# Optimization experiments

Measured on AMD Instinct MI355X. Metric: run time of the kernel, lower is better.

Reference implementation:

```python
import jax, jax.numpy as jnp
import numpy as np

EPS = 1e-8

def setup_inputs() -> dict:
    key = jax.random.key(0)
    k1, k2 = jax.random.split(key)
    B, IN, OUT, G = 32768, 256, 256, 5
    x = jax.random.normal(k1, (B, IN), dtype=jnp.float32)
    grid = jnp.linspace(-1.0, 1.0, G).astype(jnp.float32)
    coef = jax.random.normal(k2, (OUT, IN, G), dtype=jnp.float32) * 0.1
    scale = jnp.ones((OUT, IN), dtype=jnp.float32)
    bias = jnp.zeros((OUT,), dtype=jnp.float32)
    return {"x": x, "grid": grid, "coef": coef, "scale": scale, "bias": bias}

def reference(x, grid, coef, scale, bias):
    # global min-max normalization to [-1, 1]
    xmin, xmax = x.min(), x.max()
    xn = 2.0 * (x - xmin) / (xmax - xmin + EPS) - 1.0
    # cubic bump B-spline-like basis: (batch, in, grid)
    dist = jnp.abs(xn[..., None] - grid)
    basis = jnp.where(dist < 1.0, 1.0 - dist ** 3, 0.0)
    basis = basis / (basis.sum(axis=-1, keepdims=True) + EPS)
    # fused contraction over (in, grid); equals ((basis*coef).sum(-1)*scale).sum(-1)
    w = coef * scale[..., None]          # (out, in, grid)
    out = jnp.einsum('big,oig->bo', basis, w) + bias
    return out
```

## Files before the change

kernel.cpp:

```cpp
#include <hip/hip_runtime.h>
#include <stdint.h>


#define B_SZ   32768
#define IN_SZ  256
#define OUT_SZ 256
#define EPSF   1e-8f

typedef __bf16 bf16x8 __attribute__((ext_vector_type(8)));
typedef unsigned short ushort8 __attribute__((ext_vector_type(8)));
typedef float floatx16 __attribute__((ext_vector_type(16)));

union frag_u { uint4 u; bf16x8 v; };

__device__ __forceinline__ unsigned short f2bf(float f) {
  unsigned u = __float_as_uint(f);
  u += 0x7FFFu + ((u >> 16) & 1u);
  return (unsigned short)(u >> 16);
}


__global__ void __launch_bounds__(256) prep_kernel(const float* __restrict__ coef,
                                                   const float* __restrict__ scale,
                                                   const float* __restrict__ x,
                                                   unsigned short* __restrict__ wf,
                                                   float* __restrict__ part, int n4) {
  const int t = threadIdx.x;
  if (blockIdx.x < 256) {
    int idx = blockIdx.x * 256 + t;
    int o = idx >> 8, i = idx & 255;
    float s = scale[idx];
    const float* c = coef + (size_t)idx * 5;
    ushort8 v;
    v[0] = f2bf(c[0] * s); v[1] = f2bf(c[1] * s); v[2] = f2bf(c[2] * s);
    v[3] = f2bf(c[3] * s); v[4] = f2bf(c[4] * s);
    v[5] = 0; v[6] = 0; v[7] = 0;
    int chunk = (((o >> 5) * 64 + (i >> 2)) * 2 + ((i >> 1) & 1)) * 64
                + (i & 1) * 32 + (o & 31);
    *(ushort8*)(wf + (size_t)chunk * 8) = v;
  } else {
    int mb = blockIdx.x - 256;
    const float4* x4 = (const float4*)x;
    float lmin = 1e30f, lmax = -1e30f;
    for (int i = mb * 256 + t; i < n4; i += 256 * 256) {
      float4 v = x4[i];
      lmin = fminf(lmin, fminf(fminf(v.x, v.y), fminf(v.z, v.w)));
      lmax = fmaxf(lmax, fmaxf(fmaxf(v.x, v.y), fmaxf(v.z, v.w)));
    }
    #pragma unroll
    for (int off = 32; off >= 1; off >>= 1) {
      lmin = fminf(lmin, __shfl_down(lmin, off, 64));
      lmax = fmaxf(lmax, __shfl_down(lmax, off, 64));
    }
    __shared__ float smn[4], smx[4];
    if ((t & 63) == 0) { smn[t >> 6] = lmin; smx[t >> 6] = lmax; }
    __syncthreads();
    if (t == 0) {
      part[2 * mb]     = fminf(fminf(smn[0], smn[1]), fminf(smn[2], smn[3]));
      part[2 * mb + 1] = fmaxf(fmaxf(smx[0], smx[1]), fmaxf(smx[2], smx[3]));
    }
  }
}

__device__ __forceinline__ bf16x8 basisfrag(float xval, float scA, float scB) {
  float xn = fmaf(xval, scA, scB);
  float d0 = xn + 1.0f, d1 = xn + 0.5f, d3 = xn - 0.5f, d4 = xn - 1.0f;
  float b0 = fmaxf(fmaf(d0 * d0, -fabsf(d0), 1.0f), 0.0f);
  float b1 = fmaxf(fmaf(d1 * d1, -fabsf(d1), 1.0f), 0.0f);
  float b2 = fmaxf(fmaf(xn * xn, -fabsf(xn), 1.0f), 0.0f);
  float b3 = fmaxf(fmaf(d3 * d3, -fabsf(d3), 1.0f), 0.0f);
  float b4 = fmaxf(fmaf(d4 * d4, -fabsf(d4), 1.0f), 0.0f);
  float sum = ((b0 + b1) + (b2 + b3)) + b4;
  float inv = __builtin_amdgcn_rcpf(sum);
  b0 *= inv; b1 *= inv; b2 *= inv; b3 *= inv; b4 *= inv;
  frag_u r;
  r.u.x = __builtin_amdgcn_perm(__float_as_uint(b1), __float_as_uint(b0), 0x07060302u);
  r.u.y = __builtin_amdgcn_perm(__float_as_uint(b3), __float_as_uint(b2), 0x07060302u);
  r.u.z = __float_as_uint(b4) >> 16;
  r.u.w = 0u;
  return r.v;
}

__global__ void __launch_bounds__(256, 2) kan_gemm(
    const float* __restrict__ x,
    const unsigned short* __restrict__ wf,
    const float* __restrict__ bias,
    const float* __restrict__ part,
    float* __restrict__ out)
{
  __shared__ __align__(16) unsigned short Bb[2][16384];
  __shared__ float2 red[4];

  const int t = threadIdx.x;
  const int lane = t & 63;
  const int wm = t >> 6;
  const int l31 = lane & 31, lh = lane >> 5;
  const int bRow = blockIdx.x * 128;
  const int bCol = blockIdx.y * 128;
  const int row = bRow + wm * 32 + l31;

  auto stage = [&](int c, int buf) {
    #pragma unroll
    for (int r = 0; r < 8; ++r) {
      int idx = r * 4 + wm;
      const unsigned short* src = wf +
          ((size_t)(((blockIdx.y * 4 + (idx >> 3)) * 64 + (c * 4 + ((idx >> 1) & 3))) * 2
                    + (idx & 1))) * 512 + (size_t)lane * 8;
      __builtin_amdgcn_global_load_lds(
          (const __attribute__((address_space(1))) unsigned int*)src,
          (__attribute__((address_space(3))) unsigned int*)(&Bb[buf][idx * 512 + lane * 8]),
          16, 0, 0);
    }
  };

  const float* xrow = x + (size_t)row * IN_SZ;

  stage(0, 0);
  float4 xq[4], xqn[4];
  #pragma unroll
  for (int g = 0; g < 4; ++g) xq[g] = *(const float4*)(xrow + g * 4);

  float2 p = ((const float2*)part)[t];
  float mn = p.x, mx = p.y;
  #pragma unroll
  for (int off = 32; off >= 1; off >>= 1) {
    mn = fminf(mn, __shfl_down(mn, off, 64));
    mx = fmaxf(mx, __shfl_down(mx, off, 64));
  }
  if (lane == 0) red[wm] = make_float2(mn, mx);
  __syncthreads();
  mn = fminf(fminf(red[0].x, red[1].x), fminf(red[2].x, red[3].x));
  mx = fmaxf(fmaxf(red[0].y, red[1].y), fmaxf(red[2].y, red[3].y));
  const float scA = 2.0f / (mx - mn + EPSF);
  const float scB = -mn * scA - 1.0f;

  floatx16 acc[4] = {};
  bf16x8 br[2][8];

  auto ldsB = [&](int ktr, int buf, bf16x8* dst) {
    #pragma unroll
    for (int q = 0; q < 8; ++q) {
      int ni = q >> 1, ks = q & 1;
      dst[q] = *(const bf16x8*)(&Bb[buf][((ni * 4 + ktr) * 2 + ks) * 512 + lane * 8]);
    }
  };

  for (int c = 0; c < 16; ++c) {
    const int buf = c & 1;

    __syncthreads();

    if (c < 15) {
      stage(c + 1, buf ^ 1);
      #pragma unroll
      for (int g = 0; g < 4; ++g)
        xqn[g] = *(const float4*)(xrow + (c + 1) * 16 + g * 4);
    }

    ldsB(0, buf, br[0]);

    #pragma unroll
    for (int ktr = 0; ktr < 4; ++ktr) {
      if (ktr < 3) ldsB(ktr + 1, buf, br[(ktr + 1) & 1]);

      float xv0 = lh ? xq[ktr].y : xq[ktr].x;
      float xv1 = lh ? xq[ktr].w : xq[ktr].z;
      bf16x8 af0 = basisfrag(xv0, scA, scB);
      bf16x8 af1 = basisfrag(xv1, scA, scB);

      bf16x8* B = br[ktr & 1];
      #pragma unroll
      for (int ni = 0; ni < 4; ++ni)
        acc[ni] = __builtin_amdgcn_mfma_f32_32x32x16_bf16(af0, B[ni * 2 + 0], acc[ni], 0, 0, 0);
      #pragma unroll
      for (int ni = 0; ni < 4; ++ni)
        acc[ni] = __builtin_amdgcn_mfma_f32_32x32x16_bf16(af1, B[ni * 2 + 1], acc[ni], 0, 0, 0);
    }

    if (c < 15) {
      #pragma unroll
      for (int g = 0; g < 4; ++g) xq[g] = xqn[g];
    }
  }

  #pragma unroll
  for (int ni = 0; ni < 4; ++ni) {
    int o = bCol + ni * 32 + l31;
    float bs = bias[o];
    int rb = bRow + wm * 32 + 4 * lh;
    #pragma unroll
    for (int reg = 0; reg < 16; ++reg) {
      int r = rb + (reg & 3) + 8 * (reg >> 2);
      out[(size_t)r * OUT_SZ + o] = acc[ni][reg] + bs;
    }
  }
}

extern "C" void kernel_launch(void* const* d_in, const int* in_sizes, int n_in,
                              void* d_out, int out_size, void* d_ws, size_t ws_size,
                              hipStream_t stream) {
  const float* x     = (const float*)d_in[0];
  const float* coef  = (const float*)d_in[2];
  const float* scale = (const float*)d_in[3];
  const float* bias  = (const float*)d_in[4];
  float* out = (float*)d_out;

  size_t need = 4096 + (size_t)OUT_SZ * IN_SZ * 8 * 2;
  if (ws_size < need) return;

  float* part = (float*)d_ws;
  unsigned short* wf = (unsigned short*)((char*)d_ws + 4096);

  prep_kernel<<<512, 256, 0, stream>>>(coef, scale, x, wf, part,
                                       (B_SZ * IN_SZ) / 4);
  dim3 g(B_SZ / 128, OUT_SZ / 128);
  kan_gemm<<<g, 256, 0, stream>>>(x, wf, bias, part, out);
}
```

Before: 136.4 us.

## Split the K dimension across two blocks and combine results with atomic adds

```diff
diff --git a/kernel.cpp b/kernel.cpp
--- a/kernel.cpp
+++ b/kernel.cpp
@@ -81,14 +81,14 @@
   return r.v;
 }
 
-__global__ void __launch_bounds__(256, 2) kan_gemm(
+__global__ void __launch_bounds__(256, 4) kan_gemm(
     const float* __restrict__ x,
     const unsigned short* __restrict__ wf,
     const float* __restrict__ bias,
     const float* __restrict__ part,
     float* __restrict__ out)
 {
-  __shared__ __align__(16) unsigned short Bb[2][16384];
+  __shared__ __align__(16) unsigned short Bb[2][8192];
   __shared__ float2 red[4];
 
   const int t = threadIdx.x;
@@ -97,15 +97,17 @@
   const int l31 = lane & 31, lh = lane >> 5;
   const int bRow = blockIdx.x * 128;
   const int bCol = blockIdx.y * 128;
-  const int row = bRow + wm * 32 + l31;
+  const int kb   = blockIdx.z;
+  const int row  = bRow + wm * 32 + l31;
 
   auto stage = [&](int c, int buf) {
     #pragma unroll
-    for (int r = 0; r < 8; ++r) {
+    for (int r = 0; r < 4; ++r) {
       int idx = r * 4 + wm;
+      int ktg = kb * 32 + c * 2 + ((idx >> 1) & 1);
       const unsigned short* src = wf +
-          ((size_t)(((blockIdx.y * 4 + (idx >> 3)) * 64 + (c * 4 + ((idx >> 1) & 3))) * 2
-                    + (idx & 1))) * 512 + (size_t)lane * 8;
+          ((size_t)(((blockIdx.y * 4 + (idx >> 2)) * 64 + ktg) * 2 + (idx & 1))) * 512
+          + (size_t)lane * 8;
       __builtin_amdgcn_global_load_lds(
           (const __attribute__((address_space(1))) unsigned int*)src,
           (__attribute__((address_space(3))) unsigned int*)(&Bb[buf][idx * 512 + lane * 8]),
@@ -113,12 +115,12 @@
     }
   };
 
-  const float* xrow = x + (size_t)row * IN_SZ;
+  const float* xrow = x + (size_t)row * IN_SZ + kb * 128;
 
   stage(0, 0);
-  float4 xq[4], xqn[4];
-  #pragma unroll
-  for (int g = 0; g < 4; ++g) xq[g] = *(const float4*)(xrow + g * 4);
+  float4 xq[2], xqn[2];
+  xq[0] = *(const float4*)(xrow + 0);
+  xq[1] = *(const float4*)(xrow + 4);
 
   float2 p = ((const float2*)part)[t];
   float mn = p.x, mx = p.y;
@@ -135,15 +137,6 @@
   const float scB = -mn * scA - 1.0f;
 
   floatx16 acc[4] = {};
-  bf16x8 br[2][8];
-
-  auto ldsB = [&](int ktr, int buf, bf16x8* dst) {
-    #pragma unroll
-    for (int q = 0; q < 8; ++q) {
-      int ni = q >> 1, ks = q & 1;
-      dst[q] = *(const bf16x8*)(&Bb[buf][((ni * 4 + ktr) * 2 + ks) * 512 + lane * 8]);
-    }
-  };
 
   for (int c = 0; c < 16; ++c) {
     const int buf = c & 1;
@@ -152,46 +145,42 @@
 
     if (c < 15) {
       stage(c + 1, buf ^ 1);
-      #pragma unroll
-      for (int g = 0; g < 4; ++g)
-        xqn[g] = *(const float4*)(xrow + (c + 1) * 16 + g * 4);
-    }
-
-    ldsB(0, buf, br[0]);
-
-    #pragma unroll
-    for (int ktr = 0; ktr < 4; ++ktr) {
-      if (ktr < 3) ldsB(ktr + 1, buf, br[(ktr + 1) & 1]);
-
+      xqn[0] = *(const float4*)(xrow + (c + 1) * 8);
+      xqn[1] = *(const float4*)(xrow + (c + 1) * 8 + 4);
+    }
+
+    #pragma unroll
+    for (int ktr = 0; ktr < 2; ++ktr) {
       float xv0 = lh ? xq[ktr].y : xq[ktr].x;
       float xv1 = lh ? xq[ktr].w : xq[ktr].z;
       bf16x8 af0 = basisfrag(xv0, scA, scB);
       bf16x8 af1 = basisfrag(xv1, scA, scB);
 
-      bf16x8* B = br[ktr & 1];
       #pragma unroll
-      for (int ni = 0; ni < 4; ++ni)
-        acc[ni] = __builtin_amdgcn_mfma_f32_32x32x16_bf16(af0, B[ni * 2 + 0], acc[ni], 0, 0, 0);
+      for (int ni = 0; ni < 4; ++ni) {
+        bf16x8 b0 = *(const bf16x8*)(&Bb[buf][((ni * 2 + ktr) * 2 + 0) * 512 + lane * 8]);
+        acc[ni] = __builtin_amdgcn_mfma_f32_32x32x16_bf16(af0, b0, acc[ni], 0, 0, 0);
+      }
       #pragma unroll
-      for (int ni = 0; ni < 4; ++ni)
-        acc[ni] = __builtin_amdgcn_mfma_f32_32x32x16_bf16(af1, B[ni * 2 + 1], acc[ni], 0, 0, 0);
-    }
-
-    if (c < 15) {
-      #pragma unroll
-      for (int g = 0; g < 4; ++g) xq[g] = xqn[g];
-    }
+      for (int ni = 0; ni < 4; ++ni) {
+        bf16x8 b1 = *(const bf16x8*)(&Bb[buf][((ni * 2 + ktr) * 2 + 1) * 512 + lane * 8]);
+        acc[ni] = __builtin_amdgcn_mfma_f32_32x32x16_bf16(af1, b1, acc[ni], 0, 0, 0);
+      }
+    }
+
+    xq[0] = xqn[0];
+    xq[1] = xqn[1];
   }
 
   #pragma unroll
   for (int ni = 0; ni < 4; ++ni) {
     int o = bCol + ni * 32 + l31;
-    float bs = bias[o];
+    float bs = (kb == 0) ? bias[o] : 0.0f;
     int rb = bRow + wm * 32 + 4 * lh;
     #pragma unroll
     for (int reg = 0; reg < 16; ++reg) {
       int r = rb + (reg & 3) + 8 * (reg >> 2);
-      out[(size_t)r * OUT_SZ + o] = acc[ni][reg] + bs;
+      atomicAdd(&out[(size_t)r * OUT_SZ + o], acc[ni][reg] + bs);
     }
   }
 }
@@ -211,8 +200,9 @@
   float* part = (float*)d_ws;
   unsigned short* wf = (unsigned short*)((char*)d_ws + 4096);
 
+  hipMemsetAsync(d_out, 0, (size_t)B_SZ * OUT_SZ * sizeof(float), stream);
   prep_kernel<<<512, 256, 0, stream>>>(coef, scale, x, wf, part,
                                        (B_SZ * IN_SZ) / 4);
-  dim3 g(B_SZ / 128, OUT_SZ / 128);
+  dim3 g(B_SZ / 128, OUT_SZ / 128, 2);
   kan_gemm<<<g, 256, 0, stream>>>(x, wf, bias, part, out);
 }
```

Measured after the change: 172.3 us. 26.4% more time.
